# Kernel optimization log

Hardware: AMD Instinct MI355X
Metric: run time of the kernel (lower is better)

## Reference

```python
import jax, jax.numpy as jnp
import numpy as np

WS = 8          # window_size
SHIFT = WS // 2 # shift for 'SW' type
HEADS = 6
HD = 32


def setup_inputs() -> dict:
    key = jax.random.key(0)
    ks = jax.random.split(key, 6)
    return {
        "x": jax.random.normal(ks[0], (4, 256, 256, 192), jnp.float32),
        "w_qkv": jax.random.normal(ks[1], (192, 576), jnp.float32) * 0.02,
        "b_qkv": jax.random.normal(ks[2], (576,), jnp.float32) * 0.02,
        "rel_pos": jax.random.normal(ks[3], (HEADS, 2 * WS - 1, 2 * WS - 1), jnp.float32) * 0.02,
        "w_out": jax.random.normal(ks[4], (192, 192), jnp.float32) * 0.02,
        "b_out": jax.random.normal(ks[5], (192,), jnp.float32) * 0.02,
    }


def reference(x, w_qkv, b_qkv, rel_pos, w_out, b_out):
    b, h, w, c = x.shape
    scale = HD ** (-0.5)
    wa = WS * WS  # window area
    # shifted-window roll
    x = jnp.roll(x, (-SHIFT, -SHIFT), axis=(1, 2))
    hw, ww = h // WS, w // WS
    nw = hw * ww
    # partition into windows: [b, nw, wa, c]
    xw = x.reshape(b, hw, WS, ww, WS, c).transpose(0, 1, 3, 2, 4, 5).reshape(b, nw, wa, c)
    qkv = xw @ w_qkv + b_qkv                       # [b, nw, wa, 3c]
    qkv = qkv.reshape(b, nw, wa, 3, HEADS, HD)
    q = qkv[..., 0, :, :] * scale
    k = qkv[..., 1, :, :]
    v = qkv[..., 2, :, :]
    attn = jnp.einsum('bnqhd,bnkhd->bnhqk', q, k)  # [b, nw, heads, wa, wa]
    # relative position bias
    coords = jnp.stack(jnp.meshgrid(jnp.arange(WS), jnp.arange(WS), indexing='ij')).reshape(2, -1).T  # [wa,2]
    rel = coords[:, None, :] - coords[None, :, :] + WS - 1   # [wa, wa, 2]
    bias = rel_pos[:, rel[..., 0], rel[..., 1]]              # [heads, wa, wa]
    attn = attn + bias[None, None]
    # shift mask (only last window masked, per the module's generate_mask)
    s = WS - SHIFT
    mask = jnp.zeros((nw, wa, wa), bool)
    mask = mask.at[-1, :s, s:].set(True).at[-1, s:, :s].set(True)
    attn = jnp.where(mask[None, :, None], -jnp.inf, attn)
    attn = jax.nn.softmax(attn, axis=-1)
    out = jnp.einsum('bnhqk,bnkhd->bnqhd', attn, v)          # [b, nw, wa, heads, hd]
    out = out.reshape(b, hw, ww, WS, WS, c).transpose(0, 1, 3, 2, 4, 5).reshape(b, h, w, c)
    out = out @ w_out + b_out
    out = jnp.roll(out, (SHIFT, SHIFT), axis=(1, 2))
    return out
```

## Files before the change

### kernel.cpp

```cpp
#include <hip/hip_runtime.h>
#include <hip/hip_bf16.h>

typedef __attribute__((ext_vector_type(8))) short short8;
typedef __attribute__((ext_vector_type(4))) float f32x4;

#define MFMA(a, b, c) __builtin_amdgcn_mfma_f32_16x16x32_bf16((a), (b), (c), 0, 0, 0)

namespace {
constexpr int IMG = 256;
constexpr int NWIN = 1024;
constexpr float SCALE = 0.17677669529663687f;
constexpr float L2E   = 1.4426950408889634f;
}

__device__ __forceinline__ unsigned pack2(float a, float b) {
    __hip_bfloat162 h = __float22bfloat162_rn(make_float2(a, b));
    union { __hip_bfloat162 h; unsigned u; } v; v.h = h;
    return v.u;
}

__global__ __launch_bounds__(256) void to_bf16_T(const float* __restrict__ in,
                                                 unsigned short* __restrict__ out,
                                                 int K, int N, int scale_n, float scale) {
    __shared__ float tile[32][65];
    const int t = threadIdx.x;
    const int nb = blockIdx.x * 64, kb = blockIdx.y * 32;
    const int tn = t & 63, tk = t >> 6;
#pragma unroll
    for (int p = 0; p < 8; ++p)
        tile[p * 4 + tk][tn] = in[(size_t)(kb + p * 4 + tk) * N + nb + tn];
    __syncthreads();
    const int n = t >> 2, kc = (t & 3) * 8;
    const float s = (nb + n) < scale_n ? scale : 1.0f;
    uint4 u;
    u.x = pack2(tile[kc + 0][n] * s, tile[kc + 1][n] * s);
    u.y = pack2(tile[kc + 2][n] * s, tile[kc + 3][n] * s);
    u.z = pack2(tile[kc + 4][n] * s, tile[kc + 5][n] * s);
    u.w = pack2(tile[kc + 6][n] * s, tile[kc + 7][n] * s);
    *(uint4*)(out + (size_t)(nb + n) * K + kb + kc) = u;
}

__global__ __launch_bounds__(256) void build_bias(const float* __restrict__ rel_pos,
                                                  const float* __restrict__ b_qkv,
                                                  float* __restrict__ biasf,
                                                  float* __restrict__ bq2) {
    const int o = blockIdx.x * 256 + threadIdx.x;
    const int k = o & 63, q = (o >> 6) & 63, h = o >> 12;
    const int qy = q >> 3, qx = q & 7, ky = k >> 3, kx = k & 7;
    const float bv = rel_pos[h * 225 + (qy - ky + 7) * 15 + (qx - kx + 7)] * L2E;
    biasf[o] = bv;
    const bool masked = (q < 4) != (k < 4);
    biasf[24576 + o] = masked ? -30000.0f : bv;
    if (blockIdx.x == 0) {
        for (int i = threadIdx.x; i < 576; i += 256)
            bq2[i] = b_qkv[i] * (i < 192 ? SCALE : 1.0f);
    }
}

__global__ __launch_bounds__(256, 3)
void qkv_attn(const float* __restrict__ x,
              const float* __restrict__ bq2,
              const float* __restrict__ biasf,
              const unsigned short* __restrict__ wqT,
              unsigned short* __restrict__ oh_ws) {
    __shared__ unsigned short x_s[64][200];
    __shared__ unsigned short qp_s[64][72];
    __shared__ unsigned short kp_s[64][72];
    __shared__ unsigned short vT_s[64][72];

    const int tid = threadIdx.x;
    const int w   = tid >> 6;
    const int l   = tid & 63;
    const int l15 = l & 15, lg = l >> 4;
    const int wing = blockIdx.x;
    const int b   = wing >> 10;
    const int win = wing & (NWIN - 1);
    const int wy  = win >> 5, wx = win & 31;
    const float* bias_t = biasf + ((win == NWIN - 1) ? 24576 : 0);

    {
        const int t  = tid >> 2;
        const int c0 = tid & 3;
        const int pr = ((wy << 3) + (t >> 3) + 4) & (IMG - 1);
        const int pc = ((wx << 3) + (t & 7) + 4) & (IMG - 1);
        const float* xrow = x + ((size_t)((b * IMG + pr) * IMG + pc)) * 192;
#pragma unroll
        for (int i = 0; i < 12; ++i) {
            const int c = c0 + 4 * i;
            const float4 xv = *reinterpret_cast<const float4*>(xrow + c * 4);
            uint2 pk; pk.x = pack2(xv.x, xv.y); pk.y = pack2(xv.z, xv.w);
            *(uint2*)(&x_s[t][c * 4]) = pk;
        }
    }
    __syncthreads();

    const int h_loc = w >> 1;
    const int qt0   = 2 * (w & 1);

#pragma unroll 1
    for (int g = 0; g < 3; ++g) {
        f32x4 aq[3][4];
        const unsigned short* wp[3];
#pragma unroll
        for (int ci = 0; ci < 3; ++ci) {
            const int t = w + 4 * ci;
            const int which = t >> 2, sub = t & 3;
            const int hh = sub >> 1, d0 = (sub & 1) * 16;
            const int grow = which * 192 + (2 * g + hh) * 32 + d0 + l15;
            wp[ci] = wqT + (size_t)grow * 192 + lg * 8;
            f32x4 c0;
            if (which < 2) {
                const float4 b4 = *reinterpret_cast<const float4*>(
                    bq2 + which * 192 + (2 * g + hh) * 32 + d0 + 4 * lg);
                c0 = f32x4{b4.x, b4.y, b4.z, b4.w};
            } else {
                const float bb = bq2[384 + (2 * g + hh) * 32 + d0 + l15];
                c0 = f32x4{bb, bb, bb, bb};
            }
#pragma unroll
            for (int nt = 0; nt < 4; ++nt) aq[ci][nt] = c0;
        }

        __builtin_amdgcn_s_setprio(1);
#pragma unroll
        for (int ks = 0; ks < 6; ++ks) {
            short8 xf[4];
#pragma unroll
            for (int nt = 0; nt < 4; ++nt)
                xf[nt] = *(const short8*)(&x_s[16 * nt + l15][ks * 32 + lg * 8]);
#pragma unroll
            for (int ci = 0; ci < 3; ++ci) {
                const short8 wf = *(const short8*)wp[ci];
                wp[ci] += 32;
                if (ci < 2 ? ((w + 4 * ci) >> 2) < 2 : ((w + 8) >> 2) < 2) {
#pragma unroll
                    for (int nt = 0; nt < 4; ++nt) aq[ci][nt] = MFMA(wf, xf[nt], aq[ci][nt]);
                } else {
#pragma unroll
                    for (int nt = 0; nt < 4; ++nt) aq[ci][nt] = MFMA(xf[nt], wf, aq[ci][nt]);
                }
            }
        }
        __builtin_amdgcn_s_setprio(0);

#pragma unroll
        for (int ci = 0; ci < 3; ++ci) {
            const int t = w + 4 * ci;
            const int which = t >> 2, sub = t & 3;
            const int hh = sub >> 1, d0 = (sub & 1) * 16;
            if (which < 2) {
                const int rbase = hh * 32 + d0 + 4 * lg;
#pragma unroll
                for (int nt = 0; nt < 4; ++nt) {
                    const int tok = 16 * nt + l15;
                    uint2 pk;
                    pk.x = pack2(aq[ci][nt][0], aq[ci][nt][1]);
                    pk.y = pack2(aq[ci][nt][2], aq[ci][nt][3]);
                    if (which == 0) *(uint2*)(&qp_s[tok][rbase]) = pk;
                    else            *(uint2*)(&kp_s[tok][rbase]) = pk;
                }
            } else {
                const int dcol = hh * 32 + d0 + l15;
#pragma unroll
                for (int nt = 0; nt < 4; ++nt) {
                    uint2 pk;
                    pk.x = pack2(aq[ci][nt][0], aq[ci][nt][1]);
                    pk.y = pack2(aq[ci][nt][2], aq[ci][nt][3]);
                    *(uint2*)(&vT_s[dcol][16 * nt + 4 * lg]) = pk;
                }
            }
        }
        __syncthreads();

        short8 qf[2], kf[4];
#pragma unroll
        for (int mq = 0; mq < 2; ++mq)
            qf[mq] = *(const short8*)(&qp_s[16 * (qt0 + mq) + l15][h_loc * 32 + lg * 8]);
#pragma unroll
        for (int nt = 0; nt < 4; ++nt)
            kf[nt] = *(const short8*)(&kp_s[16 * nt + l15][h_loc * 32 + lg * 8]);
        f32x4 s[2][4];
        const f32x4 z = {0.f, 0.f, 0.f, 0.f};
        __builtin_amdgcn_s_setprio(1);
#pragma unroll
        for (int mq = 0; mq < 2; ++mq)
#pragma unroll
            for (int nt = 0; nt < 4; ++nt) s[mq][nt] = MFMA(kf[nt], qf[mq], z);
        __builtin_amdgcn_s_setprio(0);
        __syncthreads();

        unsigned short (*p_buf)[72] = (h_loc == 0) ? qp_s : kp_s;
        const int h = 2 * g + h_loc;
        float ri[2];
#pragma unroll
        for (int mq = 0; mq < 2; ++mq) {
            const int q = 16 * (qt0 + mq) + l15;
            const float* bq = bias_t + ((h * 64 + q) << 6) + 4 * lg;
            float e[4][4], sum = 0.f;
#pragma unroll
            for (int nt = 0; nt < 4; ++nt) {
                const float4 bb = *(const float4*)(bq + 16 * nt);
                e[nt][0] = __builtin_exp2f(fmaf(s[mq][nt][0], L2E, bb.x));
                e[nt][1] = __builtin_exp2f(fmaf(s[mq][nt][1], L2E, bb.y));
                e[nt][2] = __builtin_exp2f(fmaf(s[mq][nt][2], L2E, bb.z));
                e[nt][3] = __builtin_exp2f(fmaf(s[mq][nt][3], L2E, bb.w));
                sum += (e[nt][0] + e[nt][1]) + (e[nt][2] + e[nt][3]);
            }
            sum += __shfl_xor(sum, 16);
            sum += __shfl_xor(sum, 32);
            ri[mq] = __builtin_amdgcn_rcpf(sum);
#pragma unroll
            for (int nt = 0; nt < 4; ++nt) {
                uint2 pk;
                pk.x = pack2(e[nt][0], e[nt][1]);
                pk.y = pack2(e[nt][2], e[nt][3]);
                *(uint2*)(&p_buf[q][16 * nt + 4 * lg]) = pk;
            }
        }

        f32x4 o[2][2];
#pragma unroll
        for (int dm = 0; dm < 2; ++dm)
#pragma unroll
            for (int qn = 0; qn < 2; ++qn) o[dm][qn] = z;
        __builtin_amdgcn_s_setprio(1);
#pragma unroll
        for (int ks2 = 0; ks2 < 2; ++ks2) {
            short8 pf[2];
#pragma unroll
            for (int qn = 0; qn < 2; ++qn)
                pf[qn] = *(const short8*)(&p_buf[16 * (qt0 + qn) + l15][ks2 * 32 + lg * 8]);
#pragma unroll
            for (int dm = 0; dm < 2; ++dm) {
                const short8 vf = *(const short8*)(&vT_s[h_loc * 32 + 16 * dm + l15][ks2 * 32 + lg * 8]);
#pragma unroll
                for (int qn = 0; qn < 2; ++qn) o[dm][qn] = MFMA(vf, pf[qn], o[dm][qn]);
            }
        }
        __builtin_amdgcn_s_setprio(0);

        if (g < 2) __syncthreads();

#pragma unroll
        for (int dm = 0; dm < 2; ++dm)
#pragma unroll
            for (int qn = 0; qn < 2; ++qn) {
                const int tok = 16 * (qt0 + qn) + l15;
                const int c0 = h * 32 + 16 * dm + 4 * lg;
                const float rr = ri[qn];
                uint2 pk;
                pk.x = pack2(o[dm][qn][0] * rr, o[dm][qn][1] * rr);
                pk.y = pack2(o[dm][qn][2] * rr, o[dm][qn][3] * rr);
                *(uint2*)(oh_ws + (size_t)wing * 12288 + tok * 192 + c0) = pk;
            }
    }
}

__global__ __launch_bounds__(256, 6)
void gemm2_out(const unsigned short* __restrict__ oh_ws,
               const unsigned short* __restrict__ woT,
               const float* __restrict__ b_out,
               float* __restrict__ out) {
    __shared__ unsigned short oh_s[64][200];

    const int tid = threadIdx.x;
    const int w   = tid >> 6;
    const int l   = tid & 63;
    const int l15 = l & 15, lg = l >> 4;
    const int wing = blockIdx.x;
    const int b   = wing >> 10;
    const int win = wing & (NWIN - 1);
    const int wy  = win >> 5, wx = win & 31;

#pragma unroll
    for (int it = 0; it < 6; ++it) {
        const int i = tid + 256 * it;
        const int t = i / 24, c8 = i % 24;
        const uint4 u = *(const uint4*)(oh_ws + (size_t)wing * 12288 + t * 192 + c8 * 8);
        *(uint4*)(&oh_s[t][c8 * 8]) = u;
    }
    __syncthreads();

#pragma unroll
    for (int ci = 0; ci < 3; ++ci) {
        const int oc0 = 16 * (w + 4 * ci);
        const float4 bo = *reinterpret_cast<const float4*>(b_out + oc0 + 4 * lg);
        f32x4 acc[4];
#pragma unroll
        for (int nt = 0; nt < 4; ++nt) acc[nt] = f32x4{bo.x, bo.y, bo.z, bo.w};
#pragma unroll
        for (int ks = 0; ks < 6; ++ks) {
            const short8 af = *(const short8*)(woT + (size_t)(oc0 + l15) * 192 + ks * 32 + lg * 8);
#pragma unroll
            for (int nt = 0; nt < 4; ++nt) {
                const short8 bfr = *(const short8*)(&oh_s[16 * nt + l15][ks * 32 + lg * 8]);
                acc[nt] = MFMA(af, bfr, acc[nt]);
            }
        }
#pragma unroll
        for (int nt = 0; nt < 4; ++nt) {
            const int tok = 16 * nt + l15;
            const int pr = ((wy << 3) + (tok >> 3) + 4) & (IMG - 1);
            const int pc = ((wx << 3) + (tok & 7) + 4) & (IMG - 1);
            float* orow = out + (size_t)((b * IMG + pr) * IMG + pc) * 192;
            *reinterpret_cast<float4*>(orow + oc0 + 4 * lg) =
                make_float4(acc[nt][0], acc[nt][1], acc[nt][2], acc[nt][3]);
        }
    }
}

extern "C" void kernel_launch(void* const* d_in, const int* in_sizes, int n_in,
                              void* d_out, int out_size, void* d_ws, size_t ws_size,
                              hipStream_t stream) {
    (void)in_sizes; (void)n_in; (void)out_size; (void)ws_size;
    const float* x       = (const float*)d_in[0];
    const float* w_qkv   = (const float*)d_in[1];
    const float* b_qkv   = (const float*)d_in[2];
    const float* rel_pos = (const float*)d_in[3];
    const float* w_out   = (const float*)d_in[4];
    const float* b_out   = (const float*)d_in[5];
    float* out = (float*)d_out;

    unsigned short* wqT   = (unsigned short*)d_ws;
    unsigned short* woT   = wqT + 576 * 192;
    float*          biasf = (float*)(woT + 192 * 192);
    float*          bq2   = biasf + 2 * 24576;
    unsigned short* oh_ws = (unsigned short*)(bq2 + 576);

    to_bf16_T<<<dim3(9, 6), 256, 0, stream>>>(w_qkv, wqT, 192, 576, 192, SCALE);
    to_bf16_T<<<dim3(3, 6), 256, 0, stream>>>(w_out, woT, 192, 192, 0, 1.0f);
    build_bias<<<dim3(96), 256, 0, stream>>>(rel_pos, b_qkv, biasf, bq2);

    qkv_attn<<<dim3(4 * NWIN), dim3(256), 0, stream>>>(x, bq2, biasf, wqT, oh_ws);
    gemm2_out<<<dim3(4 * NWIN), dim3(256), 0, stream>>>(oh_ws, woT, b_out, out);
}
```

Before: 314.7 us.

## Fuse output projection into attention kernel, removing bf16 workspace round-trip

Merges the separate output-projection GEMM into the windowed attention kernel. Each head-pair's attention output is written to shared memory and immediately multiplied with the transposed output weight, and the results accumulate in registers across the three head groups. This removes the global write and re-read of the per-window attention output and one kernel launch. In exchange it adds 48 accumulator registers per thread in a kernel limited to 3 blocks per SM, plus extra barriers per group, so register pressure or spills could reduce occupancy.

```diff
diff --git a/kernel.cpp b/kernel.cpp
--- a/kernel.cpp
+++ b/kernel.cpp
@@ -58,11 +58,13 @@
 }
 
 __global__ __launch_bounds__(256, 3)
-void qkv_attn(const float* __restrict__ x,
-              const float* __restrict__ bq2,
-              const float* __restrict__ biasf,
-              const unsigned short* __restrict__ wqT,
-              unsigned short* __restrict__ oh_ws) {
+void wmsa_fused(const float* __restrict__ x,
+                const float* __restrict__ bq2,
+                const float* __restrict__ biasf,
+                const unsigned short* __restrict__ wqT,
+                const unsigned short* __restrict__ woT,
+                const float* __restrict__ b_out,
+                float* __restrict__ out) {
     __shared__ unsigned short x_s[64][200];
     __shared__ unsigned short qp_s[64][72];
     __shared__ unsigned short kp_s[64][72];
@@ -96,6 +98,15 @@
 
     const int h_loc = w >> 1;
     const int qt0   = 2 * (w & 1);
+
+    f32x4 g2[3][4];
+#pragma unroll
+    for (int mi = 0; mi < 3; ++mi) {
+        const float4 bo = *reinterpret_cast<const float4*>(b_out + 16 * (w + 4 * mi) + 4 * lg);
+        const f32x4 c0 = {bo.x, bo.y, bo.z, bo.w};
+#pragma unroll
+        for (int nt = 0; nt < 4; ++nt) g2[mi][nt] = c0;
+    }
 
 #pragma unroll 1
     for (int g = 0; g < 3; ++g) {
@@ -238,73 +249,52 @@
             }
         }
         __builtin_amdgcn_s_setprio(0);
-
-        if (g < 2) __syncthreads();
-
 #pragma unroll
         for (int dm = 0; dm < 2; ++dm)
 #pragma unroll
             for (int qn = 0; qn < 2; ++qn) {
                 const int tok = 16 * (qt0 + qn) + l15;
-                const int c0 = h * 32 + 16 * dm + 4 * lg;
                 const float rr = ri[qn];
                 uint2 pk;
                 pk.x = pack2(o[dm][qn][0] * rr, o[dm][qn][1] * rr);
                 pk.y = pack2(o[dm][qn][2] * rr, o[dm][qn][3] * rr);
-                *(uint2*)(oh_ws + (size_t)wing * 12288 + tok * 192 + c0) = pk;
-            }
-    }
-}
-
-__global__ __launch_bounds__(256, 6)
-void gemm2_out(const unsigned short* __restrict__ oh_ws,
-               const unsigned short* __restrict__ woT,
-               const float* __restrict__ b_out,
-               float* __restrict__ out) {
-    __shared__ unsigned short oh_s[64][200];
-
-    const int tid = threadIdx.x;
-    const int w   = tid >> 6;
-    const int l   = tid & 63;
-    const int l15 = l & 15, lg = l >> 4;
-    const int wing = blockIdx.x;
-    const int b   = wing >> 10;
-    const int win = wing & (NWIN - 1);
-    const int wy  = win >> 5, wx = win & 31;
-
-#pragma unroll
-    for (int it = 0; it < 6; ++it) {
-        const int i = tid + 256 * it;
-        const int t = i / 24, c8 = i % 24;
-        const uint4 u = *(const uint4*)(oh_ws + (size_t)wing * 12288 + t * 192 + c8 * 8);
-        *(uint4*)(&oh_s[t][c8 * 8]) = u;
-    }
-    __syncthreads();
-
-#pragma unroll
-    for (int ci = 0; ci < 3; ++ci) {
-        const int oc0 = 16 * (w + 4 * ci);
-        const float4 bo = *reinterpret_cast<const float4*>(b_out + oc0 + 4 * lg);
-        f32x4 acc[4];
-#pragma unroll
-        for (int nt = 0; nt < 4; ++nt) acc[nt] = f32x4{bo.x, bo.y, bo.z, bo.w};
-#pragma unroll
-        for (int ks = 0; ks < 6; ++ks) {
-            const short8 af = *(const short8*)(woT + (size_t)(oc0 + l15) * 192 + ks * 32 + lg * 8);
-#pragma unroll
-            for (int nt = 0; nt < 4; ++nt) {
-                const short8 bfr = *(const short8*)(&oh_s[16 * nt + l15][ks * 32 + lg * 8]);
-                acc[nt] = MFMA(af, bfr, acc[nt]);
-            }
-        }
-#pragma unroll
-        for (int nt = 0; nt < 4; ++nt) {
-            const int tok = 16 * nt + l15;
-            const int pr = ((wy << 3) + (tok >> 3) + 4) & (IMG - 1);
-            const int pc = ((wx << 3) + (tok & 7) + 4) & (IMG - 1);
-            float* orow = out + (size_t)((b * IMG + pr) * IMG + pc) * 192;
-            *reinterpret_cast<float4*>(orow + oc0 + 4 * lg) =
-                make_float4(acc[nt][0], acc[nt][1], acc[nt][2], acc[nt][3]);
+                *(uint2*)(&p_buf[tok][16 * dm + 4 * lg]) = pk;
+            }
+        __syncthreads();
+
+        __builtin_amdgcn_s_setprio(1);
+#pragma unroll
+        for (int ks2 = 0; ks2 < 2; ++ks2) {
+            short8 bfr[4];
+#pragma unroll
+            for (int nt = 0; nt < 4; ++nt)
+                bfr[nt] = (ks2 == 0)
+                    ? *(const short8*)(&qp_s[16 * nt + l15][lg * 8])
+                    : *(const short8*)(&kp_s[16 * nt + l15][lg * 8]);
+#pragma unroll
+            for (int mi = 0; mi < 3; ++mi) {
+                const int oct = w + 4 * mi;
+                const short8 af = *(const short8*)(
+                    woT + (size_t)(16 * oct + l15) * 192 + g * 64 + ks2 * 32 + lg * 8);
+#pragma unroll
+                for (int nt = 0; nt < 4; ++nt) g2[mi][nt] = MFMA(af, bfr[nt], g2[mi][nt]);
+            }
+        }
+        __builtin_amdgcn_s_setprio(0);
+        if (g < 2) __syncthreads();
+    }
+
+#pragma unroll
+    for (int nt = 0; nt < 4; ++nt) {
+        const int tok = 16 * nt + l15;
+        const int pr = ((wy << 3) + (tok >> 3) + 4) & (IMG - 1);
+        const int pc = ((wx << 3) + (tok & 7) + 4) & (IMG - 1);
+        float* orow = out + (size_t)((b * IMG + pr) * IMG + pc) * 192;
+#pragma unroll
+        for (int mi = 0; mi < 3; ++mi) {
+            const int oc0 = 16 * (w + 4 * mi) + 4 * lg;
+            *reinterpret_cast<float4*>(orow + oc0) =
+                make_float4(g2[mi][nt][0], g2[mi][nt][1], g2[mi][nt][2], g2[mi][nt][3]);
         }
     }
 }
@@ -325,12 +315,11 @@
     unsigned short* woT   = wqT + 576 * 192;
     float*          biasf = (float*)(woT + 192 * 192);
     float*          bq2   = biasf + 2 * 24576;
-    unsigned short* oh_ws = (unsigned short*)(bq2 + 576);
 
     to_bf16_T<<<dim3(9, 6), 256, 0, stream>>>(w_qkv, wqT, 192, 576, 192, SCALE);
     to_bf16_T<<<dim3(3, 6), 256, 0, stream>>>(w_out, woT, 192, 192, 0, 1.0f);
     build_bias<<<dim3(96), 256, 0, stream>>>(rel_pos, b_qkv, biasf, bq2);
 
-    qkv_attn<<<dim3(4 * NWIN), dim3(256), 0, stream>>>(x, bq2, biasf, wqT, oh_ws);
-    gemm2_out<<<dim3(4 * NWIN), dim3(256), 0, stream>>>(oh_ws, woT, b_out, out);
-}
+    wmsa_fused<<<dim3(4 * NWIN), dim3(256), 0, stream>>>(
+        x, bq2, biasf, wqT, woT, b_out, out);
+}
```

New measurement: 283.4 us. 10.0% less time.
